# Performance work log

Hardware: AMD Instinct MI355X
Metric: run time of the kernel (lower is better)

The kernel has to match this reference:

```python
import jax, jax.numpy as jnp
import numpy as np

B = 4
HIDDEN = 256
NH, NL, NP = 8, 4, 4
DH = HIDDEN // NH
IMG = 256
SHAPES = ((64, 64), (32, 32), (16, 16), (8, 8))
CHS = (128, 256, 512, 512)
T = 3
NLAYERS = 6
S = sum(h * w for h, w in SHAPES)


def conv2d(x, w, b, pad):
    y = jax.lax.conv_general_dilated(x, w, (1, 1), [(pad, pad), (pad, pad)],
                                     dimension_numbers=('NCHW', 'OIHW', 'NCHW'))
    return y + b[None, :, None, None]


def group_norm(x, g, beta, groups=32, eps=1e-5):
    b, c, h, w = x.shape
    xg = x.reshape(b, groups, c // groups, h, w)
    mu = xg.mean((2, 3, 4), keepdims=True)
    var = ((xg - mu) ** 2).mean((2, 3, 4), keepdims=True)
    xg = (xg - mu) * jax.lax.rsqrt(var + eps)
    return xg.reshape(b, c, h, w) * g[None, :, None, None] + beta[None, :, None, None]


def layer_norm(x, g, b, eps=1e-5):
    mu = x.mean(-1, keepdims=True)
    var = ((x - mu) ** 2).mean(-1, keepdims=True)
    return (x - mu) * jax.lax.rsqrt(var + eps) * g + b


def pos_embed_sine(h, w, num_feats=128, temp=10000.0):
    # PositionEmbeddingSine with normalize=True, mask all-False
    scale = 2.0 * np.pi
    eps = 1e-6
    y = jnp.arange(1, h + 1, dtype=jnp.float32) / (h + eps) * scale
    x = jnp.arange(1, w + 1, dtype=jnp.float32) / (w + eps) * scale
    yy = jnp.broadcast_to(y[:, None], (h, w))
    xx = jnp.broadcast_to(x[None, :], (h, w))
    dim_t = temp ** (2.0 * (jnp.arange(num_feats) // 2).astype(jnp.float32) / num_feats)
    px = xx[..., None] / dim_t
    py = yy[..., None] / dim_t
    px = jnp.stack([jnp.sin(px[..., 0::2]), jnp.cos(px[..., 1::2])], -1).reshape(h, w, num_feats)
    py = jnp.stack([jnp.sin(py[..., 0::2]), jnp.cos(py[..., 1::2])], -1).reshape(h, w, num_feats)
    return jnp.concatenate([py, px], -1)  # (h, w, 2*num_feats)


def ms_deform(value, locs, attw):
    # value: (B,S,NH,DH); locs: (B,S,NH,NL,NP,2) normalized xy; attw: (B,S,NH,NL,NP)
    out = jnp.zeros((B, S, NH, DH), value.dtype)
    start = 0
    for l, (h, w) in enumerate(SHAPES):
        v = value[:, start:start + h * w]  # (B,hw,NH,DH)
        start += h * w
        gx = locs[:, :, :, l, :, 0] * w - 0.5  # grid_sample align_corners=False
        gy = locs[:, :, :, l, :, 1] * h - 0.5  # (B,S,NH,NP)
        x0 = jnp.floor(gx)
        y0 = jnp.floor(gy)
        wx1 = gx - x0
        wy1 = gy - y0
        acc = jnp.zeros((B, S, NH, NP, DH), value.dtype)
        for dy in (0, 1):
            for dx in (0, 1):
                xi = x0 + dx
                yi = y0 + dy
                wgt = (wx1 if dx else 1.0 - wx1) * (wy1 if dy else 1.0 - wy1)
                valid = ((xi >= 0) & (xi < w) & (yi >= 0) & (yi < h)).astype(value.dtype)
                xi_c = jnp.clip(xi, 0, w - 1).astype(jnp.int32)
                yi_c = jnp.clip(yi, 0, h - 1).astype(jnp.int32)
                idx = yi_c * w + xi_c  # (B,S,NH,NP)
                idx2 = idx.transpose(0, 1, 3, 2).reshape(B, S * NP, NH, 1)
                samp = jnp.take_along_axis(v, idx2, axis=1)  # (B,S*NP,NH,DH)
                samp = samp.reshape(B, S, NP, NH, DH).transpose(0, 1, 3, 2, 4)
                acc = acc + samp * (wgt * valid)[..., None]
        out = out + (acc * attw[:, :, :, l, :, None]).sum(3)
    return out.reshape(B, S, NH * DH)


def _forward(feat_t0_l0, feat_t0_l1, feat_t0_l2, feat_t0_l3,
             feat_t1_l0, feat_t1_l1, feat_t1_l2, feat_t1_l3,
             feat_t2_l0, feat_t2_l1, feat_t2_l2, feat_t2_l3,
             tfw,
             proj_w0, proj_b0, gn_g0, gn_b0,
             proj_w1, proj_b1, gn_g1, gn_b1,
             proj_w2, proj_b2, gn_g2, gn_b2,
             proj_w3, proj_b3, gn_g3, gn_b3,
             level_embed,
             off_w, off_b, aw_w, aw_b, val_w, val_b, out_w, out_b,
             ln1_g, ln1_b, ff1_w, ff1_b, ff2_w, ff2_b, ln2_g, ln2_b,
             c1_w, c1_b, c2_w, c2_b):
    feats = [[feat_t0_l0, feat_t0_l1, feat_t0_l2, feat_t0_l3],
             [feat_t1_l0, feat_t1_l1, feat_t1_l2, feat_t1_l3],
             [feat_t2_l0, feat_t2_l1, feat_t2_l2, feat_t2_l3]]
    proj = [(proj_w0, proj_b0, gn_g0, gn_b0), (proj_w1, proj_b1, gn_g1, gn_b1),
            (proj_w2, proj_b2, gn_g2, gn_b2), (proj_w3, proj_b3, gn_g3, gn_b3)]
    priors = (0, CHS[0], CHS[1], CHS[2])  # replicates original (buggy) prior indexing
    srcs, poss = [], []
    for l in range(NL):
        atf = jnp.stack([feats[t][l] for t in range(T)], 1)  # (B,T,C,H,W)
        wsl = jax.nn.softmax(tfw[:, priors[l]:priors[l] + CHS[l]], axis=0)  # (T,C)
        fused = (atf * wsl[None, :, :, None, None]).sum(1)
        pw, pb, gg, gb = proj[l]
        x = group_norm(conv2d(fused, pw, pb, 0), gg, gb)  # 1x1 proj + GN
        h, w = SHAPES[l]
        srcs.append(x.reshape(B, HIDDEN, h * w).transpose(0, 2, 1))
        pe = pos_embed_sine(h, w).reshape(h * w, HIDDEN) + level_embed[l]
        poss.append(jnp.broadcast_to(pe[None], (B, h * w, HIDDEN)))
    src = jnp.concatenate(srcs, 1)  # (B,S,256)
    pos = jnp.concatenate(poss, 1)
    # reference points (valid_ratios == 1 since masks are all False)
    refs = []
    for (h, w) in SHAPES:
        gy, gx = jnp.meshgrid((jnp.arange(h) + 0.5) / h, (jnp.arange(w) + 0.5) / w, indexing='ij')
        refs.append(jnp.stack([gx.ravel(), gy.ravel()], -1))
    ref = jnp.broadcast_to(jnp.concatenate(refs, 0)[None, :, None, :], (B, S, NL, 2)).astype(jnp.float32)
    norm_wh = jnp.array([[w, h] for (h, w) in SHAPES], jnp.float32)  # (NL,2) xy
    for i in range(NLAYERS):
        q = src + pos
        off = (q @ off_w[i].T + off_b[i]).reshape(B, S, NH, NL, NP, 2)
        aw = jax.nn.softmax((q @ aw_w[i].T + aw_b[i]).reshape(B, S, NH, NL * NP), -1).reshape(B, S, NH, NL, NP)
        val = (src @ val_w[i].T + val_b[i]).reshape(B, S, NH, DH)
        locs = ref[:, :, None, :, None, :] + off / norm_wh[None, None, None, :, None, :]
        attn = ms_deform(val, locs, aw) @ out_w[i].T + out_b[i]
        src = layer_norm(src + attn, ln1_g[i], ln1_b[i])
        ff = (jax.nn.relu(src @ ff1_w[i].T + ff1_b[i])) @ ff2_w[i].T + ff2_b[i]
        src = layer_norm(src + ff, ln2_g[i], ln2_b[i])
    h0, w0 = SHAPES[0]
    layer0 = src[:, :h0 * w0, :].reshape(B, h0, w0, HIDDEN).transpose(0, 3, 1, 2)
    pred = conv2d(jax.nn.relu(conv2d(layer0, c1_w, c1_b, 1)), c2_w, c2_b, 1)
    return jax.image.resize(pred, (B, pred.shape[1], IMG, IMG), method='bilinear')


def setup_inputs():
    key = jax.random.key(0)
    ks = iter(jax.random.split(key, 128))
    d = {}
    for t in range(T):
        for l, ((h, w), c) in enumerate(zip(SHAPES, CHS)):
            d['feat_t%d_l%d' % (t, l)] = jax.random.normal(next(ks), (B, c, h, w), jnp.float32)
    d['tfw'] = jax.random.normal(next(ks), (T, sum(CHS)), jnp.float32)
    for l, c in enumerate(CHS):
        d['proj_w%d' % l] = jax.random.normal(next(ks), (HIDDEN, c, 1, 1), jnp.float32) * 0.02
        d['proj_b%d' % l] = jnp.zeros((HIDDEN,), jnp.float32)
        d['gn_g%d' % l] = jnp.ones((HIDDEN,), jnp.float32)
        d['gn_b%d' % l] = jnp.zeros((HIDDEN,), jnp.float32)
    d['level_embed'] = jax.random.normal(next(ks), (NL, HIDDEN), jnp.float32)
    Lc = NLAYERS

    def w(shape, s=0.02):
        return jax.random.normal(next(ks), shape, jnp.float32) * s
    d['off_w'] = w((Lc, NH * NL * NP * 2, HIDDEN))
    d['off_b'] = w((Lc, NH * NL * NP * 2), 0.1)
    d['aw_w'] = w((Lc, NH * NL * NP, HIDDEN))
    d['aw_b'] = w((Lc, NH * NL * NP), 0.1)
    d['val_w'] = w((Lc, HIDDEN, HIDDEN))
    d['val_b'] = jnp.zeros((Lc, HIDDEN), jnp.float32)
    d['out_w'] = w((Lc, HIDDEN, HIDDEN))
    d['out_b'] = jnp.zeros((Lc, HIDDEN), jnp.float32)
    d['ln1_g'] = jnp.ones((Lc, HIDDEN), jnp.float32)
    d['ln1_b'] = jnp.zeros((Lc, HIDDEN), jnp.float32)
    d['ff1_w'] = w((Lc, 1024, HIDDEN))
    d['ff1_b'] = jnp.zeros((Lc, 1024), jnp.float32)
    d['ff2_w'] = w((Lc, HIDDEN, 1024))
    d['ff2_b'] = jnp.zeros((Lc, HIDDEN), jnp.float32)
    d['ln2_g'] = jnp.ones((Lc, HIDDEN), jnp.float32)
    d['ln2_b'] = jnp.zeros((Lc, HIDDEN), jnp.float32)
    d['c1_w'] = w((64, HIDDEN, 3, 3))
    d['c1_b'] = jnp.zeros((64,), jnp.float32)
    d['c2_w'] = w((2, 64, 3, 3))
    d['c2_b'] = jnp.zeros((2,), jnp.float32)
    return d


def reference(feat_t0_l0, feat_t0_l1, feat_t0_l2, feat_t0_l3,
              feat_t1_l0, feat_t1_l1, feat_t1_l2, feat_t1_l3,
              feat_t2_l0, feat_t2_l1, feat_t2_l2, feat_t2_l3,
              tfw,
              proj_w0, proj_b0, gn_g0, gn_b0,
              proj_w1, proj_b1, gn_g1, gn_b1,
              proj_w2, proj_b2, gn_g2, gn_b2,
              proj_w3, proj_b3, gn_g3, gn_b3,
              level_embed,
              off_w, off_b, aw_w, aw_b, val_w, val_b, out_w, out_b,
              ln1_g, ln1_b, ff1_w, ff1_b, ff2_w, ff2_b, ln2_g, ln2_b,
              c1_w, c1_b, c2_w, c2_b):
    return _forward(feat_t0_l0, feat_t0_l1, feat_t0_l2, feat_t0_l3,
                    feat_t1_l0, feat_t1_l1, feat_t1_l2, feat_t1_l3,
                    feat_t2_l0, feat_t2_l1, feat_t2_l2, feat_t2_l3,
                    tfw,
                    proj_w0, proj_b0, gn_g0, gn_b0,
                    proj_w1, proj_b1, gn_g1, gn_b1,
                    proj_w2, proj_b2, gn_g2, gn_b2,
                    proj_w3, proj_b3, gn_g3, gn_b3,
                    level_embed,
                    off_w, off_b, aw_w, aw_b, val_w, val_b, out_w, out_b,
                    ln1_g, ln1_b, ff1_w, ff1_b, ff2_w, ff2_b, ln2_g, ln2_b,
                    c1_w, c1_b, c2_w, c2_b)
```

## Files before the change

### kernel.cpp

```cpp
#include <hip/hip_runtime.h>
#include <math.h>

constexpr int kB = 4;
constexpr int kS = 5440;
constexpr int kH = 256;
constexpr int kNH = 8, kNL = 4, kNP = 4, kDH = 32;
constexpr int kM = kB * kS;
constexpr int kCHSUM = 1408;

typedef __attribute__((ext_vector_type(8))) short short8v;
typedef __attribute__((ext_vector_type(4))) short short4v;
typedef __attribute__((ext_vector_type(4))) float f32x4;
typedef __attribute__((ext_vector_type(16))) float f32x16;

__device__ inline short bf16rne(float f) {
    unsigned u = __float_as_uint(f);
    u += 0x7FFF + ((u >> 16) & 1);
    return (short)(u >> 16);
}
__device__ inline float bf2f(short s) {
    return __uint_as_float(((unsigned)(unsigned short)s) << 16);
}
__device__ inline int xcd_swz(int orig, int nwg) {
    int q = nwg >> 3, r = nwg & 7;
    int x = orig & 7, o = orig >> 3;
    return (x < r ? x*(q+1) : r*(q+1) + (x-r)*q) + o;
}
#define LSWZ(row, chunk) ((row)*40 + ((chunk) ^ ((row) & 24)))

__device__ inline void cv4(const float* __restrict__ in, short* __restrict__ out, int q)
{
    int i = q * 4;
    f32x4 v = *(const f32x4*)(in + i);
    short4v o;
    o[0]=bf16rne(v[0]); o[1]=bf16rne(v[1]); o[2]=bf16rne(v[2]); o[3]=bf16rne(v[3]);
    *(short4v*)(out + i) = o;
}
__global__ __launch_bounds__(256) void prep_all_kernel(
        const float* __restrict__ off_w, const float* __restrict__ aw_w,
        const float* __restrict__ off_b, const float* __restrict__ aw_b,
        const float* __restrict__ val_w, const float* __restrict__ out_w,
        const float* __restrict__ ff1w, const float* __restrict__ ff2w,
        const float* __restrict__ pw0, const float* __restrict__ pw1,
        const float* __restrict__ pw2, const float* __restrict__ pw3,
        const float* __restrict__ c1w, const float* __restrict__ c2w,
        short* __restrict__ Wcat, float* __restrict__ bcat,
        short* __restrict__ valwb, short* __restrict__ outwb,
        short* __restrict__ ff1wb, short* __restrict__ ff2wb,
        short* __restrict__ pwb, short* __restrict__ c1wb, float* __restrict__ c2wr)
{
    int idx = blockIdx.x * 256 + threadIdx.x;
    if (idx < 589824) {
        int col = idx & 255;
        int row = (idx >> 8) % 384;
        int i   = idx / (384*256);
        float v = (row < 256) ? off_w[((size_t)i*256 + row)*256 + col]
                              : aw_w[((size_t)i*128 + row-256)*256 + col];
        Wcat[idx] = bf16rne(v);
        return;
    }
    idx -= 589824;
    if (idx < 2304) {
        int row = idx % 384, i = idx / 384;
        bcat[idx] = (row < 256) ? off_b[i*256 + row] : aw_b[i*128 + row-256];
        return;
    }
    idx -= 2304;
    if (idx < 98304) { cv4(val_w, valwb, idx); return; }
    idx -= 98304;
    if (idx < 98304) { cv4(out_w, outwb, idx); return; }
    idx -= 98304;
    if (idx < 393216) { cv4(ff1w, ff1wb, idx); return; }
    idx -= 393216;
    if (idx < 393216) { cv4(ff2w, ff2wb, idx); return; }
    idx -= 393216;
    if (idx < 8192)  { cv4(pw0, pwb + 0,      idx); return; }
    idx -= 8192;
    if (idx < 16384) { cv4(pw1, pwb + 32768,  idx); return; }
    idx -= 16384;
    if (idx < 32768) { cv4(pw2, pwb + 98304,  idx); return; }
    idx -= 32768;
    if (idx < 32768) { cv4(pw3, pwb + 229376, idx); return; }
    idx -= 32768;
    if (idx < 147456) {
        int k = idx % 2304, o = idx / 2304;
        int kblk = k >> 8, c = k & 255;
        c1wb[idx] = bf16rne(c1w[(size_t)o*2304 + c*9 + kblk]);
        return;
    }
    idx -= 147456;
    if (idx < 1152) {
        int c = idx & 63, r = idx >> 6;
        int o = r / 9, kblk = r % 9;
        c2wr[idx] = c2w[((size_t)o*64 + c)*9 + kblk];
    }
}
constexpr int kPrepThreads = 589824+2304+98304+98304+393216+393216+8192+16384+32768+32768+147456+1152;


__global__ __launch_bounds__(256) void fuseT_kernel(const float* __restrict__ f0,
        const float* __restrict__ f1, const float* __restrict__ f2,
        const float* __restrict__ tfw, short* __restrict__ out,
        int c, int hw, int prior)
{
    __shared__ float tile[32][33];
    int p0 = blockIdx.x * 32;
    int c0 = blockIdx.y * 32;
    int b  = blockIdx.z;
    int tx  = threadIdx.x & 31;
    int ty8 = threadIdx.x >> 5;
    #pragma unroll
    for (int i = 0; i < 4; ++i) {
        int ch = c0 + ty8 + i*8;
        float t0 = tfw[0*kCHSUM + prior + ch];
        float t1 = tfw[1*kCHSUM + prior + ch];
        float t2 = tfw[2*kCHSUM + prior + ch];
        float m = fmaxf(t0, fmaxf(t1, t2));
        float e0 = expf(t0-m), e1 = expf(t1-m), e2 = expf(t2-m);
        float inv = 1.0f / (e0+e1+e2);
        size_t base = ((size_t)b*c + ch)*hw + p0 + tx;
        tile[ty8+i*8][tx] = f0[base]*(e0*inv) + f1[base]*(e1*inv) + f2[base]*(e2*inv);
    }
    __syncthreads();
    #pragma unroll
    for (int i = 0; i < 4; ++i) {
        int p = p0 + ty8 + i*8;
        out[((size_t)b*hw + p)*c + c0 + tx] = bf16rne(tile[tx][ty8+i*8]);
    }
}

__global__ __launch_bounds__(256) void gn_sum_kernel(const float* __restrict__ xbufT,
        float* __restrict__ gnstat, int nchunks)
{
    int chunk = blockIdx.x, b = blockIdx.y;
    int t = threadIdx.x;
    size_t base = ((size_t)b*nchunks + chunk) * 4096;
    float s = 0.f, q = 0.f;
    #pragma unroll
    for (int i = 0; i < 4; ++i) {
        f32x4 v = *(const f32x4*)(xbufT + base + i*1024 + t*4);
        s += v[0]+v[1]+v[2]+v[3];
        q += v[0]*v[0]+v[1]*v[1]+v[2]*v[2]+v[3]*v[3];
    }
    __shared__ float ls[256], lq[256];
    ls[t] = s; lq[t] = q; __syncthreads();
    if (t < 64) { ls[t] += ls[t+64]+ls[t+128]+ls[t+192];
                  lq[t] += lq[t+64]+lq[t+128]+lq[t+192]; }
    __syncthreads();
    if (t < 32) {
        float ss = ls[2*t] + ls[2*t+1];
        float qq = lq[2*t] + lq[2*t+1];
        size_t o = (((size_t)b*nchunks + chunk)*32 + t)*2;
        gnstat[o] = ss; gnstat[o+1] = qq;
    }
}

__global__ __launch_bounds__(256) void gn_fin_kernel(const float* __restrict__ gnstat,
        const float* __restrict__ gg, const float* __restrict__ gb,
        float* __restrict__ gnA, float* __restrict__ gnB, int nchunks, int hw)
{
    int b = blockIdx.x, t = threadIdx.x;
    int g = t >> 3, sub = t & 7;
    float s = 0.f, q = 0.f;
    for (int c = sub; c < nchunks; c += 8) {
        size_t o = (((size_t)b*nchunks + c)*32 + g)*2;
        s += gnstat[o]; q += gnstat[o+1];
    }
    __shared__ float ls[256], lq[256], gmu[32], ginv[32];
    ls[t] = s; lq[t] = q; __syncthreads();
    if (sub < 4) { ls[t] += ls[t+4]; lq[t] += lq[t+4]; } __syncthreads();
    if (sub < 2) { ls[t] += ls[t+2]; lq[t] += lq[t+2]; } __syncthreads();
    if (sub == 0) {
        float ss = ls[t] + ls[t+1], qq = lq[t] + lq[t+1];
        float n = 8.0f * hw;
        float mu = ss / n;
        float var = qq / n - mu*mu;
        gmu[g] = mu; ginv[g] = rsqrtf(var + 1e-5f);
    }
    __syncthreads();
    int ch = t;
    float A = ginv[ch>>3] * gg[ch];
    float B = gb[ch] - gmu[ch>>3] * A;
    gnA[b*256 + ch] = A;
    gnB[b*256 + ch] = B;
}

__global__ __launch_bounds__(256) void gn_apply_kernel(const float* __restrict__ xbufT,
        const float* __restrict__ gnA, const float* __restrict__ gnB,
        const float* __restrict__ pos, float* __restrict__ src,
        short* __restrict__ srcbf, short* __restrict__ qbf, int hw, int sbase)
{
    int E = hw * 256;
    size_t fl = (size_t)blockIdx.x*1024 + threadIdx.x*4;
    int b = (int)(fl / E);
    int off = (int)(fl - (size_t)b*E);
    int p = off >> 8, col = off & 255;
    f32x4 v = *(const f32x4*)(xbufT + fl);
    f32x4 A = *(const f32x4*)(gnA + b*256 + col);
    f32x4 Bv = *(const f32x4*)(gnB + b*256 + col);
    size_t si = ((size_t)b*kS + sbase + p)*256 + col;
    f32x4 pv = *(const f32x4*)(pos + si);
    f32x4 o;
    o[0]=v[0]*A[0]+Bv[0]; o[1]=v[1]*A[1]+Bv[1];
    o[2]=v[2]*A[2]+Bv[2]; o[3]=v[3]*A[3]+Bv[3];
    *(f32x4*)(src + si) = o;
    short4v sb, qb;
    sb[0]=bf16rne(o[0]); sb[1]=bf16rne(o[1]); sb[2]=bf16rne(o[2]); sb[3]=bf16rne(o[3]);
    qb[0]=bf16rne(o[0]+pv[0]); qb[1]=bf16rne(o[1]+pv[1]);
    qb[2]=bf16rne(o[2]+pv[2]); qb[3]=bf16rne(o[3]+pv[3]);
    *(short4v*)(srcbf + si) = sb;
    *(short4v*)(qbf + si) = qb;
}

__global__ __launch_bounds__(256) void pos_all_kernel(const float* __restrict__ lev,
                                                      float* __restrict__ pos)
{
    int idx = blockIdx.x * 256 + threadIdx.x;
    if (idx >= kS * 256) return;
    int ch = idx & 255;
    int p  = idx >> 8;
    int lvl, py, px, dim;
    if (p < 4096)      { lvl = 0; dim = 64; int l = p;        py = l >> 6; px = l & 63; }
    else if (p < 5120) { lvl = 1; dim = 32; int l = p - 4096; py = l >> 5; px = l & 31; }
    else if (p < 5376) { lvl = 2; dim = 16; int l = p - 5120; py = l >> 4; px = l & 15; }
    else               { lvl = 3; dim = 8;  int l = p - 5376; py = l >> 3; px = l & 7; }
    int c2 = ch & 127;
    int i  = c2 >> 1;
    float invdt = exp2f((float)i * -0.20762050593046015f);
    float t;
    if (ch < 128) t = (py + 1) / ((float)dim + 1e-6f) * 6.2831853071795864f;
    else          t = (px + 1) / ((float)dim + 1e-6f) * 6.2831853071795864f;
    float arg = t * invdt;
    float val = (c2 & 1) ? cosf(arg) : sinf(arg);
    val += lev[lvl*kH + ch];
    #pragma unroll
    for (int b = 0; b < kB; ++b)
        pos[(size_t)b*kS*256 + idx] = val;
}

template<int BM, int OUTMODE>
__global__ __launch_bounds__(256) void gemm32(const short* __restrict__ A,
        const short* __restrict__ W, const float* __restrict__ bias,
        float* __restrict__ C, short* __restrict__ Cb, int N, int K, int relu, int ncols)
{
    constexpr int FI = BM / 64;
    constexpr int NAV = (BM == 128) ? 4 : 2;
    __shared__ short Asm[2][BM * 40];
    __shared__ short Bsm[2][128 * 40];
    const int lin = xcd_swz(blockIdx.x, gridDim.x);
    const int bn  = (lin % ncols) * 128;
    const int bm  = (lin / ncols) * BM;
    const int t    = threadIdx.x;
    const int lane = t & 63;
    const int wid  = t >> 6;
    const int wr   = wid >> 1;
    const int wc   = wid & 1;
    const int l31  = lane & 31;
    const int hi8  = (lane >> 5) * 8;

    f32x16 acc[FI][2];
    #pragma unroll
    for (int i = 0; i < FI; ++i)
        #pragma unroll
        for (int j = 0; j < 2; ++j)
            acc[i][j] = (f32x16){0,0,0,0,0,0,0,0,0,0,0,0,0,0,0,0};

    int sa_r, sa_k;
    if constexpr (BM == 128) { sa_r = t >> 1; sa_k = (t & 1) * 32; }
    else                     { sa_r = t >> 2; sa_k = (t & 3) * 16; }
    const short* Aptr = A + (size_t)(bm + sa_r)*K + sa_k;
    const int sb_r = t >> 1;
    const int sb_k = (t & 1) * 32;
    const short* Wptr = W + (size_t)(bn + sb_r)*K + sb_k;

    short8v a[NAV], b[4];
    #pragma unroll
    for (int v = 0; v < NAV; ++v) a[v] = *(const short8v*)(Aptr + v*8);
    #pragma unroll
    for (int v = 0; v < 4; ++v)   b[v] = *(const short8v*)(Wptr + v*8);

    for (int k0 = 0; k0 < K; k0 += 64) {
        __syncthreads();
        if constexpr (BM == 128) {
            #pragma unroll
            for (int v = 0; v < 4; ++v) *(short8v*)&Asm[t & 1][LSWZ(sa_r, v*8)] = a[v];
        } else {
            #pragma unroll
            for (int v = 0; v < 2; ++v)
                *(short8v*)&Asm[sa_k >> 5][LSWZ(sa_r, (sa_k & 16) + v*8)] = a[v];
        }
        #pragma unroll
        for (int v = 0; v < 4; ++v) *(short8v*)&Bsm[t & 1][LSWZ(sb_r, v*8)] = b[v];
        __syncthreads();
        if (k0 + 64 < K) {
            #pragma unroll
            for (int v = 0; v < NAV; ++v) a[v] = *(const short8v*)(Aptr + k0 + 64 + v*8);
            #pragma unroll
            for (int v = 0; v < 4; ++v)   b[v] = *(const short8v*)(Wptr + k0 + 64 + v*8);
        }
        #pragma unroll
        for (int p = 0; p < 2; ++p)
            #pragma unroll
            for (int ks = 0; ks < 2; ++ks) {
                short8v af[FI], bfv[2];
                #pragma unroll
                for (int i = 0; i < FI; ++i)
                    af[i] = *(const short8v*)&Asm[p][LSWZ(wr*(BM/2) + i*32 + l31, ks*16 + hi8)];
                #pragma unroll
                for (int j = 0; j < 2; ++j)
                    bfv[j] = *(const short8v*)&Bsm[p][LSWZ(wc*64 + j*32 + l31, ks*16 + hi8)];
                #pragma unroll
                for (int i = 0; i < FI; ++i)
                    #pragma unroll
                    for (int j = 0; j < 2; ++j)
                        acc[i][j] = __builtin_amdgcn_mfma_f32_32x32x16_bf16(af[i], bfv[j], acc[i][j], 0, 0, 0);
            }
    }

    const int rbase = 4 * (lane >> 5);
    #pragma unroll
    for (int j = 0; j < 2; ++j) {
        int col = bn + wc*64 + j*32 + l31;
        float bz = bias[col];
        #pragma unroll
        for (int i = 0; i < FI; ++i) {
            int row0 = bm + wr*(BM/2) + i*32 + rbase;
            #pragma unroll
            for (int r = 0; r < 16; ++r) {
                int row = row0 + (r & 3) + 8*(r >> 2);
                float v = acc[i][j][r] + bz;
                if (relu) v = fmaxf(v, 0.f);
                if constexpr (OUTMODE == 0) C[(size_t)row*N + col] = v;
                else                        Cb[(size_t)row*N + col] = bf16rne(v);
            }
        }
    }
}

__global__ __launch_bounds__(256) void gemm_qv32(const short* __restrict__ Aq,
        const short* __restrict__ As, const short* __restrict__ W1,
        const short* __restrict__ W2, const float* __restrict__ b1,
        const float* __restrict__ b2, float* __restrict__ C1,
        short* __restrict__ Cb2)
{
    __shared__ short Asm[2][128 * 40];
    __shared__ short Bsm[2][128 * 40];
    const int lin = xcd_swz(blockIdx.x, gridDim.x);
    const int bn  = (lin % 5) * 128;
    const int bm  = (lin / 5) * 128;
    const bool qreg = bn < 384;
    const int K = 256;
    const int t    = threadIdx.x;
    const int lane = t & 63;
    const int wid  = t >> 6;
    const int wr   = wid >> 1;
    const int wc   = wid & 1;
    const int l31  = lane & 31;
    const int hi8  = (lane >> 5) * 8;
    const int sa_r = t >> 1;
    const int sa_p = t & 1;

    f32x16 acc[2][2];
    #pragma unroll
    for (int i = 0; i < 2; ++i)
        #pragma unroll
        for (int j = 0; j < 2; ++j)
            acc[i][j] = (f32x16){0,0,0,0,0,0,0,0,0,0,0,0,0,0,0,0};

    const short* Aptr = (qreg ? Aq : As) + (size_t)(bm + sa_r)*K + sa_p*32;
    const short* Wptr = (qreg ? (W1 + (size_t)(bn + sa_r)*K)
                              : (W2 + (size_t)(bn - 384 + sa_r)*K)) + sa_p*32;
    short8v a[4], b[4];
    #pragma unroll
    for (int v = 0; v < 4; ++v) { a[v] = *(const short8v*)(Aptr + v*8);
                                  b[v] = *(const short8v*)(Wptr + v*8); }

    for (int k0 = 0; k0 < K; k0 += 64) {
        __syncthreads();
        #pragma unroll
        for (int v = 0; v < 4; ++v) {
            *(short8v*)&Asm[sa_p][LSWZ(sa_r, v*8)] = a[v];
            *(short8v*)&Bsm[sa_p][LSWZ(sa_r, v*8)] = b[v];
        }
        __syncthreads();
        if (k0 + 64 < K) {
            #pragma unroll
            for (int v = 0; v < 4; ++v) {
                a[v] = *(const short8v*)(Aptr + k0 + 64 + v*8);
                b[v] = *(const short8v*)(Wptr + k0 + 64 + v*8);
            }
        }
        #pragma unroll
        for (int p = 0; p < 2; ++p)
            #pragma unroll
            for (int ks = 0; ks < 2; ++ks) {
                short8v af[2], bfv[2];
                #pragma unroll
                for (int i = 0; i < 2; ++i)
                    af[i] = *(const short8v*)&Asm[p][LSWZ(wr*64 + i*32 + l31, ks*16 + hi8)];
                #pragma unroll
                for (int j = 0; j < 2; ++j)
                    bfv[j] = *(const short8v*)&Bsm[p][LSWZ(wc*64 + j*32 + l31, ks*16 + hi8)];
                #pragma unroll
                for (int i = 0; i < 2; ++i)
                    #pragma unroll
                    for (int j = 0; j < 2; ++j)
                        acc[i][j] = __builtin_amdgcn_mfma_f32_32x32x16_bf16(af[i], bfv[j], acc[i][j], 0, 0, 0);
            }
    }

    const int rbase = 4 * (lane >> 5);
    if (bn == 256) {
        #pragma unroll
        for (int j = 0; j < 2; ++j) {
            int col = bn + wc*64 + j*32 + l31;
            float bz = b1[col];
            #pragma unroll
            for (int i = 0; i < 2; ++i) {
                int row0 = bm + wr*64 + i*32 + rbase;
                #pragma unroll
                for (int r = 0; r < 16; ++r) {
                    int row = row0 + (r & 3) + 8*(r >> 2);
                    float v = acc[i][j][r] + bz;
                    float m = v;
                    m = fmaxf(m, __shfl_xor(m, 1));
                    m = fmaxf(m, __shfl_xor(m, 2));
                    m = fmaxf(m, __shfl_xor(m, 4));
                    m = fmaxf(m, __shfl_xor(m, 8));
                    float e = expf(v - m);
                    float s = e;
                    s += __shfl_xor(s, 1);
                    s += __shfl_xor(s, 2);
                    s += __shfl_xor(s, 4);
                    s += __shfl_xor(s, 8);
                    C1[(size_t)row*384 + col] = e / s;
                }
            }
        }
    } else {
        #pragma unroll
        for (int j = 0; j < 2; ++j) {
            int col = bn + wc*64 + j*32 + l31;
            float bz = qreg ? b1[col] : b2[col - 384];
            #pragma unroll
            for (int i = 0; i < 2; ++i) {
                int row0 = bm + wr*64 + i*32 + rbase;
                #pragma unroll
                for (int r = 0; r < 16; ++r) {
                    int row = row0 + (r & 3) + 8*(r >> 2);
                    float v = acc[i][j][r] + bz;
                    if (qreg) C1[(size_t)row*384 + col] = v;
                    else      Cb2[(size_t)row*256 + col - 384] = bf16rne(v);
                }
            }
        }
    }
}

__global__ __launch_bounds__(256) void conv1_gemm_kernel(const short* __restrict__ srcbf,
        const short* __restrict__ Wr, const float* __restrict__ bias,
        float* __restrict__ C)
{
    __shared__ short Asm[2][128 * 40];
    __shared__ short Bsm[2][64 * 40];
    const int t    = threadIdx.x;
    const int bm   = blockIdx.x * 128;
    const int K    = 2304;
    const int lane = t & 63;
    const int wid  = t >> 6;
    const int wr   = wid >> 1;
    const int wc   = wid & 1;
    const int frow = lane & 15;
    const int g    = lane >> 4;
    const int sa_r = t >> 1;
    const int sa_p = t & 1;

    const int m  = bm + sa_r;
    const int bb = m >> 12, ys = (m >> 6) & 63, xs = m & 63;

    f32x4 acc[4][2];
    #pragma unroll
    for (int i = 0; i < 4; ++i)
        #pragma unroll
        for (int j = 0; j < 2; ++j)
            acc[i][j] = (f32x4){0.f,0.f,0.f,0.f};

    auto loadA = [&](int k0, short8v* r) {
        int kk = k0 + sa_p*32;
        int kblk = kk >> 8;
        int dyy = kblk / 3, dxx = kblk - dyy*3;
        int yy = ys + dyy - 1, xx = xs + dxx - 1;
        if (yy >= 0 && yy < 64 && xx >= 0 && xx < 64) {
            const short* p = srcbf + ((size_t)(bb*kS + yy*64 + xx))*256 + (kk & 255);
            #pragma unroll
            for (int v = 0; v < 4; ++v) r[v] = *(const short8v*)(p + v*8);
        } else {
            #pragma unroll
            for (int v = 0; v < 4; ++v) r[v] = (short8v){0,0,0,0,0,0,0,0};
        }
    };

    const int sb_r = t >> 2, sb_p = (t & 3) >> 1, sb_o = (t & 1) * 16;
    const short* Wptr = Wr + (size_t)sb_r*K + (t & 3)*16;
    short8v a[4], b[2];
    loadA(0, a);
    b[0] = *(const short8v*)Wptr;
    b[1] = *(const short8v*)(Wptr + 8);

    for (int k0 = 0; k0 < K; k0 += 64) {
        __syncthreads();
        #pragma unroll
        for (int v = 0; v < 4; ++v) *(short8v*)&Asm[sa_p][sa_r*40 + v*8] = a[v];
        *(short8v*)&Bsm[sb_p][sb_r*40 + sb_o]     = b[0];
        *(short8v*)&Bsm[sb_p][sb_r*40 + sb_o + 8] = b[1];
        __syncthreads();
        if (k0 + 64 < K) {
            loadA(k0 + 64, a);
            b[0] = *(const short8v*)(Wptr + k0 + 64);
            b[1] = *(const short8v*)(Wptr + k0 + 72);
        }
        #pragma unroll
        for (int p = 0; p < 2; ++p) {
            short8v af[4], bfv[2];
            #pragma unroll
            for (int i = 0; i < 4; ++i)
                af[i] = *(const short8v*)&Asm[p][(wr*64 + i*16 + frow)*40 + g*8];
            #pragma unroll
            for (int j = 0; j < 2; ++j)
                bfv[j] = *(const short8v*)&Bsm[p][(wc*32 + j*16 + frow)*40 + g*8];
            #pragma unroll
            for (int i = 0; i < 4; ++i)
                #pragma unroll
                for (int j = 0; j < 2; ++j)
                    acc[i][j] = __builtin_amdgcn_mfma_f32_16x16x32_bf16(af[i], bfv[j], acc[i][j], 0, 0, 0);
        }
    }

    #pragma unroll
    for (int j = 0; j < 2; ++j) {
        int col = wc*32 + j*16 + frow;
        float bz = bias[col];
        #pragma unroll
        for (int i = 0; i < 4; ++i) {
            int row = bm + wr*64 + i*16 + g*4;
            #pragma unroll
            for (int rr = 0; rr < 4; ++rr) {
                float v = fmaxf(acc[i][j][rr] + bz, 0.f);
                C[(size_t)(row + rr)*64 + col] = v;
            }
        }
    }
}

__global__ __launch_bounds__(256) void msdeform8_kernel(const short* __restrict__ val,
        const float* __restrict__ cat, short* __restrict__ msd)
{
    int blk  = xcd_swz(blockIdx.x, gridDim.x);
    int tid  = threadIdx.x;
    int d8   = tid & 3;
    int head = (tid >> 2) & 7;
    int bs   = blk*8 + (tid >> 5);
    int s  = bs % kS;
    int b  = bs / kS;
    float refx, refy;
    if (s < 4096)      { int loc = s;        refy = ((loc>>6)+0.5f)/64.f; refx = ((loc&63)+0.5f)/64.f; }
    else if (s < 5120) { int loc = s - 4096; refy = ((loc>>5)+0.5f)/32.f; refx = ((loc&31)+0.5f)/32.f; }
    else if (s < 5376) { int loc = s - 5120; refy = ((loc>>4)+0.5f)/16.f; refx = ((loc&15)+0.5f)/16.f; }
    else               { int loc = s - 5376; refy = ((loc>>3)+0.5f)/8.f;  refx = ((loc&7)+0.5f)/8.f; }
    const float* op = cat + (size_t)bs*384 + head*32;
    const float* ap = cat + (size_t)bs*384 + 256 + head*16;
    const short* vb = val + (size_t)b*kS*256 + head*32 + d8*8;
    const int WL[4] = {64,32,16,8};
    const int BASE[4] = {0,4096,5120,5376};
    float acc[8] = {0.f,0.f,0.f,0.f,0.f,0.f,0.f,0.f};
    #pragma unroll
    for (int l = 0; l < 4; ++l) {
        int wl = WL[l], base = BASE[l];
        float rxw = refx * wl - 0.5f;
        float ryw = refy * wl - 0.5f;
        f32x4 o0 = *(const f32x4*)(op + l*8);
        f32x4 o1 = *(const f32x4*)(op + l*8 + 4);
        f32x4 av = *(const f32x4*)(ap + l*4);
        float oxs[4] = {o0[0], o0[2], o1[0], o1[2]};
        float oys[4] = {o0[1], o0[3], o1[1], o1[3]};
        #pragma unroll
        for (int p = 0; p < 4; ++p) {
            float gx = rxw + oxs[p];
            float gy = ryw + oys[p];
            float x0f = floorf(gx), y0f = floorf(gy);
            float wx1 = gx - x0f, wy1 = gy - y0f;
            int x0 = (int)x0f, y0 = (int)y0f;
            float a = av[p];
            #pragma unroll
            for (int dy = 0; dy < 2; ++dy) {
                int yi = y0 + dy;
                float wy = dy ? wy1 : 1.f - wy1;
                int vyok = (yi >= 0) & (yi < wl);
                int yc = min(max(yi, 0), wl - 1);
                #pragma unroll
                for (int dx = 0; dx < 2; ++dx) {
                    int xi = x0 + dx;
                    float wx = dx ? wx1 : 1.f - wx1;
                    int vok = vyok & (xi >= 0) & (xi < wl);
                    int xc = min(max(xi, 0), wl - 1);
                    float wgt = vok ? wx*wy*a : 0.f;
                    uint4 v = *(const uint4*)&vb[(size_t)(base + yc*wl + xc)*256];
                    acc[0] = fmaf(__uint_as_float(v.x << 16),          wgt, acc[0]);
                    acc[1] = fmaf(__uint_as_float(v.x & 0xffff0000u), wgt, acc[1]);
                    acc[2] = fmaf(__uint_as_float(v.y << 16),          wgt, acc[2]);
                    acc[3] = fmaf(__uint_as_float(v.y & 0xffff0000u), wgt, acc[3]);
                    acc[4] = fmaf(__uint_as_float(v.z << 16),          wgt, acc[4]);
                    acc[5] = fmaf(__uint_as_float(v.z & 0xffff0000u), wgt, acc[5]);
                    acc[6] = fmaf(__uint_as_float(v.w << 16),          wgt, acc[6]);
                    acc[7] = fmaf(__uint_as_float(v.w & 0xffff0000u), wgt, acc[7]);
                }
            }
        }
    }
    short8v o;
    #pragma unroll
    for (int k = 0; k < 8; ++k) o[k] = bf16rne(acc[k]);
    *(short8v*)&msd[(size_t)bs*256 + head*32 + d8*8] = o;
}

template<int WQ>
__global__ __launch_bounds__(256) void add_ln_kernel(float* __restrict__ src,
        const short* __restrict__ delta, const float* __restrict__ g,
        const float* __restrict__ bta, short* __restrict__ srcbf,
        short* __restrict__ qbf, const float* __restrict__ pos)
{
    int lane = threadIdx.x & 63;
    int row  = blockIdx.x*4 + (threadIdx.x >> 6);
    f32x4* s4 = (f32x4*)(src + (size_t)row*256);
    f32x4 x = s4[lane];
    short4v dd = *(const short4v*)&delta[(size_t)row*256 + lane*4];
    x[0]+=bf2f(dd[0]); x[1]+=bf2f(dd[1]); x[2]+=bf2f(dd[2]); x[3]+=bf2f(dd[3]);
    float s = x[0]+x[1]+x[2]+x[3];
    #pragma unroll
    for (int o = 1; o < 64; o <<= 1) s += __shfl_xor(s, o);
    float mu = s * (1.f/256.f);
    f32x4 xc;
    xc[0]=x[0]-mu; xc[1]=x[1]-mu; xc[2]=x[2]-mu; xc[3]=x[3]-mu;
    float s2 = xc[0]*xc[0]+xc[1]*xc[1]+xc[2]*xc[2]+xc[3]*xc[3];
    #pragma unroll
    for (int o = 1; o < 64; o <<= 1) s2 += __shfl_xor(s2, o);
    float inv = rsqrtf(s2*(1.f/256.f) + 1e-5f);
    const f32x4 gv = ((const f32x4*)g)[lane];
    const f32x4 bv = ((const f32x4*)bta)[lane];
    f32x4 o4;
    o4[0]=xc[0]*inv*gv[0]+bv[0]; o4[1]=xc[1]*inv*gv[1]+bv[1];
    o4[2]=xc[2]*inv*gv[2]+bv[2]; o4[3]=xc[3]*inv*gv[3]+bv[3];
    s4[lane] = o4;
    short4v sb;
    sb[0]=bf16rne(o4[0]); sb[1]=bf16rne(o4[1]); sb[2]=bf16rne(o4[2]); sb[3]=bf16rne(o4[3]);
    *(short4v*)&srcbf[(size_t)row*256 + lane*4] = sb;
    if constexpr (WQ) {
        f32x4 pv = ((const f32x4*)(pos + (size_t)row*256))[lane];
        short4v qb;
        qb[0]=bf16rne(o4[0]+pv[0]); qb[1]=bf16rne(o4[1]+pv[1]);
        qb[2]=bf16rne(o4[2]+pv[2]); qb[3]=bf16rne(o4[3]+pv[3]);
        *(short4v*)&qbf[(size_t)row*256 + lane*4] = qb;
    }
}

__global__ void conv2_kernel(const float* __restrict__ c1, const float* __restrict__ w,
                             const float* __restrict__ bias, float* __restrict__ pred)
{
    int idx = blockIdx.x * blockDim.x + threadIdx.x;
    int x = idx & 63;
    int y = (idx >> 6) & 63;
    int o = (idx >> 12) & 1;
    int b = idx >> 13;
    float acc = bias[o];
    #pragma unroll
    for (int dy = 0; dy < 3; ++dy) {
        int yy = y + dy - 1;
        if (yy < 0 || yy >= 64) continue;
        #pragma unroll
        for (int dx = 0; dx < 3; ++dx) {
            int xx = x + dx - 1;
            if (xx < 0 || xx >= 64) continue;
            const f32x4* sp = (const f32x4*)(c1 + ((size_t)(b*4096) + yy*64 + xx)*64);
            const f32x4* wp = (const f32x4*)(w + (o*9 + dy*3 + dx)*64);
            #pragma unroll
            for (int c = 0; c < 16; ++c) {
                f32x4 sv = sp[c], wv = wp[c];
                acc += sv[0]*wv[0] + sv[1]*wv[1] + sv[2]*wv[2] + sv[3]*wv[3];
            }
        }
    }
    pred[idx] = acc;
}

__global__ void resize_kernel(const float* __restrict__ pred, float* __restrict__ out)
{
    int idx = blockIdx.x * blockDim.x + threadIdx.x;
    int X = idx & 255;
    int Y = (idx >> 8) & 255;
    int c = (idx >> 16) & 1;
    int b = idx >> 17;
    float sx = (X + 0.5f)*0.25f - 0.5f;
    float sy = (Y + 0.5f)*0.25f - 0.5f;
    int x0 = (int)floorf(sx); float fx = sx - x0;
    int y0 = (int)floorf(sy); float fy = sy - y0;
    int x0c = min(max(x0, 0), 63), x1c = min(max(x0+1, 0), 63);
    int y0c = min(max(y0, 0), 63), y1c = min(max(y0+1, 0), 63);
    const float* p = pred + ((size_t)(b*2 + c))*4096;
    float v00 = p[y0c*64 + x0c], v01 = p[y0c*64 + x1c];
    float v10 = p[y1c*64 + x0c], v11 = p[y1c*64 + x1c];
    out[idx] = (1.f-fy)*((1.f-fx)*v00 + fx*v01) + fy*((1.f-fx)*v10 + fx*v11);
}

extern "C" void kernel_launch(void* const* d_in, const int* in_sizes, int n_in,
                              void* d_out, int out_size, void* d_ws, size_t ws_size,
                              hipStream_t stream)
{
    const float* F[3][4];
    for (int t = 0; t < 3; ++t)
        for (int l = 0; l < 4; ++l)
            F[t][l] = (const float*)d_in[t*4 + l];
    const float* tfw = (const float*)d_in[12];
    const float *pw[4], *pb[4], *gg[4], *gb[4];
    for (int l = 0; l < 4; ++l) {
        pw[l] = (const float*)d_in[13 + 4*l];
        pb[l] = (const float*)d_in[14 + 4*l];
        gg[l] = (const float*)d_in[15 + 4*l];
        gb[l] = (const float*)d_in[16 + 4*l];
    }
    const float* lev   = (const float*)d_in[29];
    const float* off_w = (const float*)d_in[30];
    const float* off_b = (const float*)d_in[31];
    const float* aw_w  = (const float*)d_in[32];
    const float* aw_b  = (const float*)d_in[33];
    const float* val_w = (const float*)d_in[34];
    const float* val_b = (const float*)d_in[35];
    const float* out_w = (const float*)d_in[36];
    const float* out_b = (const float*)d_in[37];
    const float* ln1g  = (const float*)d_in[38];
    const float* ln1b  = (const float*)d_in[39];
    const float* ff1w  = (const float*)d_in[40];
    const float* ff1b  = (const float*)d_in[41];
    const float* ff2w  = (const float*)d_in[42];
    const float* ff2b  = (const float*)d_in[43];
    const float* ln2g  = (const float*)d_in[44];
    const float* ln2b  = (const float*)d_in[45];
    const float* c1w   = (const float*)d_in[46];
    const float* c1b   = (const float*)d_in[47];
    const float* c2w   = (const float*)d_in[48];
    const float* c2b   = (const float*)d_in[49];

    const size_t N256 = (size_t)kB * kS * 256;
    float* ws    = (float*)d_ws;
    float* src   = ws;
    short* srcbf = (short*)(src + N256);
    short* qbf   = srcbf + N256;
    short* valbf = qbf + N256;
    short* msdbf = valbf + N256;
    short* warena= msdbf + N256;
    short* Wcat_bf = warena;
    short* valw_bf = Wcat_bf + 589824;
    short* outw_bf = valw_bf + 393216;
    short* ff1w_bf = outw_bf + 393216;
    short* ff2w_bf = ff1w_bf + 1572864;
    short* pw_bf   = ff2w_bf + 1572864;
    short* c1w_bf  = pw_bf + 360448;
    float* bcat  = (float*)(c1w_bf + 147456 + 128);
    float* gnstat= bcat + 4096;
    float* gnA   = gnstat + 65536;
    float* gnB   = gnA + 1024;
    float* c2wr  = gnB + 1024;
    float* pos   = c2wr + 1280;
    float* cat   = pos + N256;
    float* tmp   = cat + (size_t)kM*384;
    short* tmpbf = (short*)tmp;
    short* ffhbf = (short*)(tmp + N256);
    short* fusedT = (short*)cat;
    float* xbufT  = tmp;
    float* c1o   = (float*)valbf;
    float* pred  = (float*)msdbf;

    const int LVL_HWS[4]  = {4096, 1024, 256, 64};
    const int LVL_BASE[4] = {0, 4096, 5120, 5376};
    const int LVL_C[4]    = {128, 256, 512, 512};
    const int LVL_PRIOR[4]= {0, 128, 256, 512};
    const int PW_OFF[4]   = {0, 32768, 98304, 229376};

    prep_all_kernel<<<(kPrepThreads + 255)/256, 256, 0, stream>>>(
        off_w, aw_w, off_b, aw_b, val_w, out_w, ff1w, ff2w,
        pw[0], pw[1], pw[2], pw[3], c1w, c2w,
        Wcat_bf, bcat, valw_bf, outw_bf, ff1w_bf, ff2w_bf, pw_bf, c1w_bf, c2wr);

    pos_all_kernel<<<(kS*256 + 255)/256, 256, 0, stream>>>(lev, pos);
    for (int l = 0; l < 4; ++l) {
        int hw = LVL_HWS[l], c = LVL_C[l];
        dim3 gf(hw/32, c/32, kB);
        fuseT_kernel<<<gf, 256, 0, stream>>>(F[0][l], F[1][l], F[2][l], tfw,
                                             fusedT, c, hw, LVL_PRIOR[l]);
        int nwg = 2 * (kB*hw/64);
        gemm32<64,0><<<nwg, 256, 0, stream>>>(fusedT, pw_bf + PW_OFF[l], pb[l],
                                              xbufT, nullptr, 256, c, 0, 2);
        int nchunks = hw / 16;
        gn_sum_kernel<<<dim3(nchunks, kB), 256, 0, stream>>>(xbufT, gnstat, nchunks);
        gn_fin_kernel<<<kB, 256, 0, stream>>>(gnstat, gg[l], gb[l], gnA, gnB, nchunks, hw);
        gn_apply_kernel<<<(kB*hw*256)/1024, 256, 0, stream>>>(xbufT, gnA, gnB, pos,
                                                              src, srcbf, qbf, hw, LVL_BASE[l]);
    }

    for (int i = 0; i < 6; ++i) {
        gemm_qv32<<<5*(kM/128), 256, 0, stream>>>(qbf, srcbf,
                Wcat_bf + (size_t)i*384*256, valw_bf + (size_t)i*65536,
                bcat + i*384, val_b + i*256, cat, valbf);
        msdeform8_kernel<<<kM/8, 256, 0, stream>>>(valbf, cat, msdbf);
        gemm32<64,1><<<2*(kM/64), 256, 0, stream>>>(msdbf, outw_bf + (size_t)i*65536,
                                                    out_b + i*256, nullptr, tmpbf, 256, 256, 0, 2);
        add_ln_kernel<0><<<kM/4, 256, 0, stream>>>(src, tmpbf, ln1g + i*256, ln1b + i*256,
                                                   srcbf, nullptr, nullptr);
        gemm32<128,1><<<8*(kM/128), 256, 0, stream>>>(srcbf, ff1w_bf + (size_t)i*262144,
                                                      ff1b + i*1024, nullptr, ffhbf, 1024, 256, 1, 8);
        gemm32<64,1><<<2*(kM/64), 256, 0, stream>>>(ffhbf, ff2w_bf + (size_t)i*262144,
                                                    ff2b + i*256, nullptr, tmpbf, 256, 1024, 0, 2);
        add_ln_kernel<1><<<kM/4, 256, 0, stream>>>(src, tmpbf, ln2g + i*256, ln2b + i*256,
                                                   srcbf, qbf, pos);
    }

    {
        conv1_gemm_kernel<<<128, 256, 0, stream>>>(srcbf, c1w_bf, c1b, c1o);
        conv2_kernel<<<(kB*2*64*64)/256, 256, 0, stream>>>(c1o, c2wr, c2b, pred);
        resize_kernel<<<(kB*2*256*256)/256, 256, 0, stream>>>(pred, (float*)d_out);
    }
}
```

Baseline: 1.100 ms.

## Store value projection in zero-padded per-level layout to drop bilinear bounds checks

The value projection epilogue now scatters rows through a lookup table into a zero-bordered padded buffer, one padded grid per level. The deformable sampling kernel can then clamp indices into the padded grid and drop the per-corner validity masks and weight selects. Out-of-range samples read zeros from the border instead of being masked. The last layer also skips writing the query/pos output it no longer needs. The cost is a scattered store in the GEMM epilogue, a larger value buffer, and a one-time zero fill in the prep kernel.

Result: faster. 1.069 ms (-2.9%).

```diff
diff --git a/kernel.cpp b/kernel.cpp
--- a/kernel.cpp
+++ b/kernel.cpp
@@ -7,6 +7,8 @@
 constexpr int kNH = 8, kNL = 4, kNP = 4, kDH = 32;
 constexpr int kM = kB * kS;
 constexpr int kCHSUM = 1408;
+constexpr int kPad = 5936;
+constexpr int kPadShorts = kB * kPad * 256;
 
 typedef __attribute__((ext_vector_type(8))) short short8v;
 typedef __attribute__((ext_vector_type(4))) short short4v;
@@ -47,7 +49,8 @@
         short* __restrict__ Wcat, float* __restrict__ bcat,
         short* __restrict__ valwb, short* __restrict__ outwb,
         short* __restrict__ ff1wb, short* __restrict__ ff2wb,
-        short* __restrict__ pwb, short* __restrict__ c1wb, float* __restrict__ c2wr)
+        short* __restrict__ pwb, short* __restrict__ c1wb, float* __restrict__ c2wr,
+        int* __restrict__ msdlut, short* __restrict__ valpad)
 {
     int idx = blockIdx.x * 256 + threadIdx.x;
     if (idx < 589824) {
@@ -93,9 +96,29 @@
         int c = idx & 63, r = idx >> 6;
         int o = r / 9, kblk = r % 9;
         c2wr[idx] = c2w[((size_t)o*64 + c)*9 + kblk];
-    }
-}
-constexpr int kPrepThreads = 589824+2304+98304+98304+393216+393216+8192+16384+32768+32768+147456+1152;
+        return;
+    }
+    idx -= 1152;
+    if (idx < kM) {
+        int bs = idx;
+        int b = bs / kS;
+        int s = bs - b*kS;
+        int pbase, wl2, py, px;
+        if (s < 4096)      { pbase = 0;    wl2 = 66; int lo = s;        py = lo>>6; px = lo&63; }
+        else if (s < 5120) { pbase = 4356; wl2 = 34; int lo = s - 4096; py = lo>>5; px = lo&31; }
+        else if (s < 5376) { pbase = 5512; wl2 = 18; int lo = s - 5120; py = lo>>4; px = lo&15; }
+        else               { pbase = 5836; wl2 = 10; int lo = s - 5376; py = lo>>3; px = lo&7; }
+        msdlut[bs] = b*kPad + pbase + (py+1)*wl2 + (px+1);
+        return;
+    }
+    idx -= kM;
+    if (idx < kPadShorts/8) {
+        short8v z = (short8v){0,0,0,0,0,0,0,0};
+        *(short8v*)(valpad + (size_t)idx*8) = z;
+    }
+}
+constexpr int kPrepThreads = 589824+2304+98304+98304+393216+393216+8192+16384+32768+32768+147456+1152
+                           + kM + kPadShorts/8;
 
 
 __global__ __launch_bounds__(256) void fuseT_kernel(const float* __restrict__ f0,
@@ -341,7 +364,7 @@
         const short* __restrict__ As, const short* __restrict__ W1,
         const short* __restrict__ W2, const float* __restrict__ b1,
         const float* __restrict__ b2, float* __restrict__ C1,
-        short* __restrict__ Cb2)
+        short* __restrict__ Cb2, const int* __restrict__ msdlut)
 {
     __shared__ short Asm[2][128 * 40];
     __shared__ short Bsm[2][128 * 40];
@@ -437,20 +460,34 @@
                 }
             }
         }
-    } else {
+    } else if (qreg) {
         #pragma unroll
         for (int j = 0; j < 2; ++j) {
             int col = bn + wc*64 + j*32 + l31;
-            float bz = qreg ? b1[col] : b2[col - 384];
+            float bz = b1[col];
             #pragma unroll
             for (int i = 0; i < 2; ++i) {
                 int row0 = bm + wr*64 + i*32 + rbase;
                 #pragma unroll
                 for (int r = 0; r < 16; ++r) {
                     int row = row0 + (r & 3) + 8*(r >> 2);
-                    float v = acc[i][j][r] + bz;
-                    if (qreg) C1[(size_t)row*384 + col] = v;
-                    else      Cb2[(size_t)row*256 + col - 384] = bf16rne(v);
+                    C1[(size_t)row*384 + col] = acc[i][j][r] + bz;
+                }
+            }
+        }
+    } else {
+        #pragma unroll
+        for (int j = 0; j < 2; ++j) {
+            int col = bn + wc*64 + j*32 + l31 - 384;
+            float bz = b2[col];
+            #pragma unroll
+            for (int i = 0; i < 2; ++i) {
+                int row0 = bm + wr*64 + i*32 + rbase;
+                #pragma unroll
+                for (int r = 0; r < 16; ++r) {
+                    int row = row0 + (r & 3) + 8*(r >> 2);
+                    int prow = msdlut[row];
+                    Cb2[(size_t)prow*256 + col] = bf16rne(acc[i][j][r] + bz);
                 }
             }
         }
@@ -552,7 +589,7 @@
     }
 }
 
-__global__ __launch_bounds__(256) void msdeform8_kernel(const short* __restrict__ val,
+__global__ __launch_bounds__(256) void msdeform8_kernel(const short* __restrict__ valpad,
         const float* __restrict__ cat, short* __restrict__ msd)
 {
     int blk  = xcd_swz(blockIdx.x, gridDim.x);
@@ -569,13 +606,14 @@
     else               { int loc = s - 5376; refy = ((loc>>3)+0.5f)/8.f;  refx = ((loc&7)+0.5f)/8.f; }
     const float* op = cat + (size_t)bs*384 + head*32;
     const float* ap = cat + (size_t)bs*384 + 256 + head*16;
-    const short* vb = val + (size_t)b*kS*256 + head*32 + d8*8;
-    const int WL[4] = {64,32,16,8};
-    const int BASE[4] = {0,4096,5120,5376};
+    const short* vb = valpad + (size_t)b*kPad*256 + head*32 + d8*8;
+    const int WL[4]  = {64,32,16,8};
+    const int WL2[4] = {66,34,18,10};
+    const int PB[4]  = {0,4356,5512,5836};
     float acc[8] = {0.f,0.f,0.f,0.f,0.f,0.f,0.f,0.f};
     #pragma unroll
     for (int l = 0; l < 4; ++l) {
-        int wl = WL[l], base = BASE[l];
+        int wl = WL[l], wl2 = WL2[l], base = PB[l];
         float rxw = refx * wl - 0.5f;
         float ryw = refy * wl - 0.5f;
         f32x4 o0 = *(const f32x4*)(op + l*8);
@@ -589,22 +627,17 @@
             float gy = ryw + oys[p];
             float x0f = floorf(gx), y0f = floorf(gy);
             float wx1 = gx - x0f, wy1 = gy - y0f;
-            int x0 = (int)x0f, y0 = (int)y0f;
+            int x1 = (int)x0f + 1, y1 = (int)y0f + 1;
             float a = av[p];
             #pragma unroll
             for (int dy = 0; dy < 2; ++dy) {
-                int yi = y0 + dy;
-                float wy = dy ? wy1 : 1.f - wy1;
-                int vyok = (yi >= 0) & (yi < wl);
-                int yc = min(max(yi, 0), wl - 1);
+                int yp = min(max(y1 + dy, 0), wl + 1);
+                float wya = (dy ? wy1 : 1.f - wy1) * a;
                 #pragma unroll
                 for (int dx = 0; dx < 2; ++dx) {
-                    int xi = x0 + dx;
-                    float wx = dx ? wx1 : 1.f - wx1;
-                    int vok = vyok & (xi >= 0) & (xi < wl);
-                    int xc = min(max(xi, 0), wl - 1);
-                    float wgt = vok ? wx*wy*a : 0.f;
-                    uint4 v = *(const uint4*)&vb[(size_t)(base + yc*wl + xc)*256];
+                    int xp = min(max(x1 + dx, 0), wl + 1);
+                    float wgt = (dx ? wx1 : 1.f - wx1) * wya;
+                    uint4 v = *(const uint4*)&vb[(size_t)(base + yp*wl2 + xp)*256];
                     acc[0] = fmaf(__uint_as_float(v.x << 16),          wgt, acc[0]);
                     acc[1] = fmaf(__uint_as_float(v.x & 0xffff0000u), wgt, acc[1]);
                     acc[2] = fmaf(__uint_as_float(v.y << 16),          wgt, acc[2]);
@@ -754,8 +787,8 @@
     float* src   = ws;
     short* srcbf = (short*)(src + N256);
     short* qbf   = srcbf + N256;
-    short* valbf = qbf + N256;
-    short* msdbf = valbf + N256;
+    short* valpad= qbf + N256;
+    short* msdbf = valpad + kPadShorts;
     short* warena= msdbf + N256;
     short* Wcat_bf = warena;
     short* valw_bf = Wcat_bf + 589824;
@@ -769,14 +802,15 @@
     float* gnA   = gnstat + 65536;
     float* gnB   = gnA + 1024;
     float* c2wr  = gnB + 1024;
-    float* pos   = c2wr + 1280;
+    int*   msdlut= (int*)(c2wr + 1280);
+    float* pos   = (float*)(msdlut + 22016);
     float* cat   = pos + N256;
     float* tmp   = cat + (size_t)kM*384;
     short* tmpbf = (short*)tmp;
     short* ffhbf = (short*)(tmp + N256);
     short* fusedT = (short*)cat;
     float* xbufT  = tmp;
-    float* c1o   = (float*)valbf;
+    float* c1o   = (float*)valpad;
     float* pred  = (float*)msdbf;
 
     const int LVL_HWS[4]  = {4096, 1024, 256, 64};
@@ -788,7 +822,8 @@
     prep_all_kernel<<<(kPrepThreads + 255)/256, 256, 0, stream>>>(
         off_w, aw_w, off_b, aw_b, val_w, out_w, ff1w, ff2w,
         pw[0], pw[1], pw[2], pw[3], c1w, c2w,
-        Wcat_bf, bcat, valw_bf, outw_bf, ff1w_bf, ff2w_bf, pw_bf, c1w_bf, c2wr);
+        Wcat_bf, bcat, valw_bf, outw_bf, ff1w_bf, ff2w_bf, pw_bf, c1w_bf, c2wr,
+        msdlut, valpad);
 
     pos_all_kernel<<<(kS*256 + 255)/256, 256, 0, stream>>>(lev, pos);
     for (int l = 0; l < 4; ++l) {
@@ -809,8 +844,8 @@
     for (int i = 0; i < 6; ++i) {
         gemm_qv32<<<5*(kM/128), 256, 0, stream>>>(qbf, srcbf,
                 Wcat_bf + (size_t)i*384*256, valw_bf + (size_t)i*65536,
-                bcat + i*384, val_b + i*256, cat, valbf);
-        msdeform8_kernel<<<kM/8, 256, 0, stream>>>(valbf, cat, msdbf);
+                bcat + i*384, val_b + i*256, cat, valpad, msdlut);
+        msdeform8_kernel<<<kM/8, 256, 0, stream>>>(valpad, cat, msdbf);
         gemm32<64,1><<<2*(kM/64), 256, 0, stream>>>(msdbf, outw_bf + (size_t)i*65536,
                                                     out_b + i*256, nullptr, tmpbf, 256, 256, 0, 2);
         add_ln_kernel<0><<<kM/4, 256, 0, stream>>>(src, tmpbf, ln1g + i*256, ln1b + i*256,
@@ -819,8 +854,12 @@
                                                       ff1b + i*1024, nullptr, ffhbf, 1024, 256, 1, 8);
         gemm32<64,1><<<2*(kM/64), 256, 0, stream>>>(ffhbf, ff2w_bf + (size_t)i*262144,
                                                     ff2b + i*256, nullptr, tmpbf, 256, 1024, 0, 2);
-        add_ln_kernel<1><<<kM/4, 256, 0, stream>>>(src, tmpbf, ln2g + i*256, ln2b + i*256,
-                                                   srcbf, qbf, pos);
+        if (i < 5)
+            add_ln_kernel<1><<<kM/4, 256, 0, stream>>>(src, tmpbf, ln2g + i*256, ln2b + i*256,
+                                                       srcbf, qbf, pos);
+        else
+            add_ln_kernel<0><<<kM/4, 256, 0, stream>>>(src, tmpbf, ln2g + i*256, ln2b + i*256,
+                                                       srcbf, nullptr, nullptr);
     }
 
     {
```
